# Kernel tuning notes

Measured on AMD Instinct MI355X. Metric: run time of the kernel, lower is better.

## Reference

```python
import jax, jax.numpy as jnp
import numpy as np

H, D = 8, 64          # num_heads, head_dim
DM = 512              # model/feature dim for q,k,v,pos
B, N, M = 8, 1024, 1024


def relative_shift(x):
    # x: [B, H, N, M] -> Transformer-XL pad/reshape shift trick
    b, h, n, m = x.shape
    x = jnp.pad(x, ((0, 0), (0, 0), (0, 0), (1, 0)))      # [B,H,N,M+1]
    x = x.reshape(b, h, m + 1, n)
    x = x[:, :, 1:, :].reshape(b, h, n, m)
    return x


def setup_inputs() -> dict:
    key = jax.random.key(0)
    ks = jax.random.split(key, 11)
    s = 0.05  # small init scale for numerical stability (glorot-ish)
    return {
        "query": jax.random.normal(ks[0], (B, N, DM), jnp.float32),
        "key": jax.random.normal(ks[1], (B, M, DM), jnp.float32),
        "value": jax.random.normal(ks[2], (B, M, DM), jnp.float32),
        "pos": jax.random.normal(ks[3], (B, M, DM), jnp.float32),
        "query_kernel": jax.random.normal(ks[4], (H, DM, D), jnp.float32) * s,
        "key_kernel": jax.random.normal(ks[5], (H, DM, D), jnp.float32) * s,
        "value_kernel": jax.random.normal(ks[6], (H, DM, D), jnp.float32) * s,
        "pos_kernel": jax.random.normal(ks[7], (H, DM, D), jnp.float32) * s,
        "projection_kernel": jax.random.normal(ks[8], (H, D, DM), jnp.float32) * s,
        "pos_bias_u": jax.random.normal(ks[9], (H, D), jnp.float32) * s,
        "pos_bias_v": jax.random.normal(ks[10], (H, D), jnp.float32) * s,
    }


def reference(query, key, value, pos, query_kernel, key_kernel, value_kernel,
              pos_kernel, projection_kernel, pos_bias_u, pos_bias_v):
    # per-head projections
    q = jnp.einsum("bni,hid->bnhd", query, query_kernel)
    k = jnp.einsum("bmi,hid->bmhd", key, key_kernel)
    v = jnp.einsum("bmi,hid->bmhd", value, value_kernel)
    p = jnp.einsum("bmi,hid->bmhd", pos, pos_kernel)

    q_u = q + pos_bias_u  # broadcast [H,D] over [B,N,H,D]
    q_v = q + pos_bias_v

    logits_u = jnp.einsum("bnhd,bmhd->bhnm", q_u, k)
    logits_v = relative_shift(jnp.einsum("bnhd,bmhd->bhnm", q_v, p))

    m = logits_u.shape[3]
    logits = (logits_u + logits_v[:, :, :, :m]) / jnp.sqrt(
        jnp.asarray(D, logits_u.dtype))

    attn = jax.nn.softmax(logits, axis=-1)            # [B,H,N,M]
    ctx = jnp.einsum("bhnm,bmhd->bnhd", attn, v)      # [B,N,H,D]
    out = jnp.einsum("bnhd,hdo->bno", ctx, projection_kernel)
    return out
```

## Files before the change

kernel.cpp:

```cpp
#include <hip/hip_runtime.h>
#include <hip/hip_bf16.h>
#include <math.h>

#define SB 8
#define SS 1024
#define SDM 512
#define SH 8
#define SD 64

typedef unsigned short ushort;
typedef __attribute__((ext_vector_type(8))) short bf16x8;
typedef __attribute__((ext_vector_type(4))) float f32x4;

#define MFMA16(a, b, c) __builtin_amdgcn_mfma_f32_16x16x32_bf16(a, b, c, 0, 0, 0)

static __device__ __forceinline__ ushort f2b(float f) {
    union { float f; unsigned u; } v; v.f = f;
    unsigned r = v.u + 0x7FFF + ((v.u >> 16) & 1);
    return (ushort)(r >> 16);
}

static __device__ __forceinline__ void gll16(const void* g, void* l) {
    __builtin_amdgcn_global_load_lds(
        (const __attribute__((address_space(1))) unsigned int*)g,
        (__attribute__((address_space(3))) unsigned int*)l, 16, 0, 0);
}

__global__ __launch_bounds__(256) void convert_x_kernel(
    const float* __restrict__ q, const float* __restrict__ k,
    const float* __restrict__ v, const float* __restrict__ p,
    ushort* __restrict__ xbf)
{
    const int which = blockIdx.y;
    const float* src = (which == 0) ? q : (which == 1) ? k : (which == 2) ? v : p;
    ushort* dst = xbf + (size_t)which * ((size_t)SB * SS * SDM);
    size_t i = ((size_t)blockIdx.x * 256 + threadIdx.x) * 8;
    float4 a = *(const float4*)(src + i);
    float4 b = *(const float4*)(src + i + 4);
    union { ushort u[8]; uint4 v4; } o;
    o.u[0] = f2b(a.x); o.u[1] = f2b(a.y); o.u[2] = f2b(a.z); o.u[3] = f2b(a.w);
    o.u[4] = f2b(b.x); o.u[5] = f2b(b.y); o.u[6] = f2b(b.z); o.u[7] = f2b(b.w);
    *(uint4*)(dst + i) = o.v4;
}

__global__ __launch_bounds__(256) void convert_w_kernel(
    const float* __restrict__ qw, const float* __restrict__ kw,
    const float* __restrict__ vw, const float* __restrict__ pw,
    const float* __restrict__ projw, ushort* __restrict__ wt)
{
    const int which = blockIdx.y;
    const int idx = blockIdx.x * 256 + threadIdx.x;
    const int c  = idx >> 9;
    const int kk = idx & 511;
    float val;
    if (which < 4) {
        const float* W = (which == 0) ? qw : (which == 1) ? kw : (which == 2) ? vw : pw;
        const int h = c >> 6, d = c & 63;
        val = W[(size_t)h * SDM * SD + (size_t)kk * SD + d];
    } else {
        val = projw[(size_t)kk * SDM + c];
    }
    wt[(size_t)which * SDM * SDM + (size_t)c * SDM + kk] = f2b(val);
}

__global__ __launch_bounds__(256) void projmm_kernel(
    const ushort* __restrict__ xbf, const ushort* __restrict__ wt,
    const float* __restrict__ bias_u, const float* __restrict__ bias_v,
    ushort* __restrict__ quo, ushort* __restrict__ qvo,
    ushort* __restrict__ ko, ushort* __restrict__ po,
    ushort* __restrict__ vto)
{
    __shared__ ushort Asm[128 * 32];
    __shared__ ushort Bsm[128 * 32];

    const int tid  = threadIdx.x;
    const int wave = tid >> 6, lane = tid & 63;
    const int quad = lane >> 4, l15 = lane & 15;
    const int which = blockIdx.z;
    const int row0 = blockIdx.x * 128;
    const int col0 = blockIdx.y * 128;
    const int wr = wave >> 1, wc = wave & 1;

    const ushort* A  = xbf + (size_t)which * ((size_t)SB * SS * SDM) + (size_t)row0 * SDM;
    const ushort* Bw = wt  + (size_t)which * (SDM * SDM) + (size_t)col0 * SDM;

    f32x4 acc[4][4];
#pragma unroll
    for (int i = 0; i < 4; ++i)
#pragma unroll
        for (int j = 0; j < 4; ++j) acc[i][j] = (f32x4){0.f, 0.f, 0.f, 0.f};

    for (int k0 = 0; k0 < SDM; k0 += 32) {
#pragma unroll
        for (int j = 0; j < 2; ++j) {
            int t = j * 256 + tid;
            int r = t >> 2, kp = (t & 3) * 8;
            gll16(A  + (size_t)r * SDM + k0 + kp, (char*)Asm + t * 16);
            gll16(Bw + (size_t)r * SDM + k0 + kp, (char*)Bsm + t * 16);
        }
        __syncthreads();

        bf16x8 af[4], bfr[4];
#pragma unroll
        for (int mt = 0; mt < 4; ++mt)
            af[mt] = *(const bf16x8*)&Asm[(wr * 64 + mt * 16 + l15) * 32 + quad * 8];
#pragma unroll
        for (int nt = 0; nt < 4; ++nt)
            bfr[nt] = *(const bf16x8*)&Bsm[(wc * 64 + nt * 16 + l15) * 32 + quad * 8];
#pragma unroll
        for (int mt = 0; mt < 4; ++mt)
#pragma unroll
            for (int nt = 0; nt < 4; ++nt)
                acc[mt][nt] = MFMA16(af[mt], bfr[nt], acc[mt][nt]);
        __syncthreads();
    }

    const float SC = 0.125f;
#pragma unroll
    for (int nt = 0; nt < 4; ++nt) {
        const int C = col0 + wc * 64 + nt * 16 + l15;
        const int h = C >> 6, d = C & 63;
        if (which == 0) {
            const float bu = bias_u[C];
            const float bv = bias_v[C];
#pragma unroll
            for (int mt = 0; mt < 4; ++mt) {
                const int Rb = row0 + wr * 64 + mt * 16 + quad * 4;
                const int b = Rb >> 10;
                const int n = Rb & 1023;
                const size_t base = ((size_t)(b * SH + h) * SS + n) * SD + d;
#pragma unroll
                for (int r = 0; r < 4; ++r) {
                    quo[base + (size_t)r * SD] = f2b((acc[mt][nt][r] + bu) * SC);
                    qvo[base + (size_t)r * SD] = f2b((acc[mt][nt][r] + bv) * SC);
                }
            }
        } else if (which == 1 || which == 3) {
            ushort* out = (which == 1) ? ko : po;
#pragma unroll
            for (int mt = 0; mt < 4; ++mt) {
                const int Rb = row0 + wr * 64 + mt * 16 + quad * 4;
                const int b = Rb >> 10;
                const int n = Rb & 1023;
                const size_t base = ((size_t)(b * SH + h) * SS + n) * SD + d;
#pragma unroll
                for (int r = 0; r < 4; ++r)
                    out[base + (size_t)r * SD] = f2b(acc[mt][nt][r]);
            }
        } else {
#pragma unroll
            for (int mt = 0; mt < 4; ++mt) {
                const int Rb = row0 + wr * 64 + mt * 16 + quad * 4;
                const int b = Rb >> 10;
                const int n = Rb & 1023;
                union { ushort u[4]; uint2 v2; } pk;
#pragma unroll
                for (int r = 0; r < 4; ++r) pk.u[r] = f2b(acc[mt][nt][r]);
                const size_t base = (size_t)(b * SH + h) * SS * SD
                                  + ((size_t)((n >> 6) * 64 + d)) * 64 + (n & 63);
                *(uint2*)&vto[base] = pk.v2;
            }
        }
    }
}

static __device__ __forceinline__ bf16x8 sfrag(const ushort* buf, int row, int seg) {
    return *(const bf16x8*)&buf[(size_t)row * 64 + ((seg ^ (row & 7)) * 8)];
}

__global__ __launch_bounds__(256) void attn_kernel(
    const ushort* __restrict__ qu, const ushort* __restrict__ qv,
    const ushort* __restrict__ kk, const ushort* __restrict__ pp,
    const ushort* __restrict__ vt, ushort* __restrict__ ctx)
{
    __shared__ ushort Kb[64 * 64];
    __shared__ ushort Pb[128 * 64];
    __shared__ float  Glds[4][16][80];
    __shared__ ushort Plds[4][16][72];

    const int tid  = threadIdx.x;
    const int wave = tid >> 6;
    const int lane = tid & 63;
    const int quad = lane >> 4;
    const int l15  = lane & 15;

    const int id   = blockIdx.x;
    const int xcd  = id & 7;
    const int slot = id >> 3;
    const int bhid = xcd * 8 + (slot >> 4);
    const int nt   = slot & 15;
    const int b    = bhid >> 3;
    const int h    = bhid & 7;
    const int n0   = nt * 64;

    const size_t bh   = (size_t)(b * SH + h);
    const ushort* qu_bh = qu + bh * SS * SD;
    const ushort* qv_bh = qv + bh * SS * SD;
    const ushort* k_bh  = kk + bh * SS * SD;
    const ushort* p_bh  = pp + bh * SS * SD;
    const ushort* vt_bh = vt + bh * SS * SD;

    const int mcD = n0 >> 6;

    const int arow  = n0 + wave * 16 + l15;
    const int arow2 = (arow + 1 < SS) ? arow + 1 : SS - 1;

    bf16x8 a_u0  = *(const bf16x8*)(qu_bh + (size_t)arow  * SD + quad * 8);
    bf16x8 a_u1  = *(const bf16x8*)(qu_bh + (size_t)arow  * SD + quad * 8 + 32);
    bf16x8 a_vl0 = *(const bf16x8*)(qv_bh + (size_t)arow  * SD + quad * 8);
    bf16x8 a_vl1 = *(const bf16x8*)(qv_bh + (size_t)arow  * SD + quad * 8 + 32);
    bf16x8 a_vu0 = *(const bf16x8*)(qv_bh + (size_t)arow2 * SD + quad * 8);
    bf16x8 a_vu1 = *(const bf16x8*)(qv_bh + (size_t)arow2 * SD + quad * 8 + 32);

    float lsum[4] = {0.f, 0.f, 0.f, 0.f};
    f32x4 O[4];
#pragma unroll
    for (int dt = 0; dt < 4; ++dt) O[dt] = (f32x4){0.f, 0.f, 0.f, 0.f};

    float  (*Gl)[80] = Glds[wave];
    ushort (*Pl)[72] = Plds[wave];

    auto stage = [&](int mc) {
        const int m0s = mc * 64;
        const int cb  = (mc <= mcD) ? (m0s - n0 + 960) : (m0s - n0 - 65);
#pragma unroll
        for (int it = 0; it < 2; ++it) {
            int t = it * 256 + tid;
            int r = t >> 3, s = t & 7;
            gll16(k_bh + (size_t)(m0s + r) * 64 + ((s ^ (r & 7)) * 8),
                  (char*)Kb + t * 16);
        }
#pragma unroll
        for (int it = 0; it < 4; ++it) {
            int t = it * 256 + tid;
            int r = t >> 3, s = t & 7;
            int c = cb + r; c = (c < 0) ? 0 : (c > SS - 1 ? SS - 1 : c);
            gll16(p_bh + (size_t)c * 64 + ((s ^ (r & 7)) * 8),
                  (char*)Pb + t * 16);
        }
    };

    stage(0);

    for (int mc = 0; mc < 16; ++mc) {
        const int m0 = mc * 64;
        const int diff = m0 - n0;
        const bool lowerband = (mc <= mcD);

        __syncthreads();

        f32x4 S[4];
#pragma unroll
        for (int mt = 0; mt < 4; ++mt) {
            const int r = mt * 16 + l15;
            f32x4 c = (f32x4){0.f, 0.f, 0.f, 0.f};
            c = MFMA16(a_u0, sfrag(Kb, r, quad), c);
            c = MFMA16(a_u1, sfrag(Kb, r, quad + 4), c);
            S[mt] = c;
        }

        float sv[4][4];
#pragma unroll
        for (int mt = 0; mt < 4; ++mt)
#pragma unroll
            for (int r = 0; r < 4; ++r) sv[mt][r] = 0.f;

        {
            const bf16x8 av0 = lowerband ? a_vl0 : a_vu0;
            const bf16x8 av1 = lowerband ? a_vl1 : a_vu1;
#pragma unroll
            for (int ti = 0; ti < 5; ++ti) {
                const int t = (3 - wave + ti) * 16 + l15;
                f32x4 g = (f32x4){0.f, 0.f, 0.f, 0.f};
                g = MFMA16(av0, sfrag(Pb, t, quad), g);
                g = MFMA16(av1, sfrag(Pb, t, quad + 4), g);
#pragma unroll
                for (int r = 0; r < 4; ++r)
                    Gl[quad * 4 + r][ti * 16 + l15] = g[r];
            }
#pragma unroll
            for (int mt = 0; mt < 4; ++mt) {
                const int mloc = mt * 16 + l15;
#pragma unroll
                for (int r = 0; r < 4; ++r) {
                    const int q4r = quad * 4 + r;
                    const int d1 = diff + mloc - (wave * 16 + q4r);
                    const bool use = lowerband ? (d1 <= 0) : (d1 >= 2);
                    if (use) sv[mt][r] = Gl[q4r][mloc - q4r + 15];
                }
            }
        }

        if (mc == mcD) {
            const int cbase = diff - 65;
            bf16x8 pu0[5], pu1[5];
#pragma unroll
            for (int ti = 0; ti < 5; ++ti) {
                int t = (3 - wave + ti) * 16 + l15;
                int c = cbase + t;
                c = (c < 0) ? 0 : (c > SS - 1 ? SS - 1 : c);
                const ushort* pr = p_bh + (size_t)c * SD + quad * 8;
                pu0[ti] = *(const bf16x8*)pr;
                pu1[ti] = *(const bf16x8*)(pr + 32);
            }
#pragma unroll
            for (int ti = 0; ti < 5; ++ti) {
                f32x4 g = (f32x4){0.f, 0.f, 0.f, 0.f};
                g = MFMA16(a_vu0, pu0[ti], g);
                g = MFMA16(a_vu1, pu1[ti], g);
#pragma unroll
                for (int r = 0; r < 4; ++r)
                    Gl[quad * 4 + r][ti * 16 + l15] = g[r];
            }
#pragma unroll
            for (int mt = 0; mt < 4; ++mt) {
                const int mloc = mt * 16 + l15;
#pragma unroll
                for (int r = 0; r < 4; ++r) {
                    const int q4r = quad * 4 + r;
                    const int d1 = diff + mloc - (wave * 16 + q4r);
                    if (d1 >= 2) sv[mt][r] = Gl[q4r][mloc - q4r + 15];
                }
            }
        }

        __syncthreads();
        if (mc + 1 < 16) stage(mc + 1);

        bf16x8 vb0[4], vb1[4];
#pragma unroll
        for (int dt = 0; dt < 4; ++dt) {
            const ushort* vp = vt_bh + (size_t)(m0 + dt * 16 + l15) * 64 + quad * 8;
            vb0[dt] = *(const bf16x8*)vp;
            vb1[dt] = *(const bf16x8*)(vp + 32);
        }

        float e[4][4];
#pragma unroll
        for (int mt = 0; mt < 4; ++mt)
#pragma unroll
            for (int r = 0; r < 4; ++r) {
                e[mt][r] = __expf(S[mt][r] + sv[mt][r]);
                lsum[r] += e[mt][r];
            }

#pragma unroll
        for (int mt = 0; mt < 4; ++mt)
#pragma unroll
            for (int r = 0; r < 4; ++r)
                Pl[quad * 4 + r][mt * 16 + l15] = f2b(e[mt][r]);

        bf16x8 ap0 = *(const bf16x8*)&Pl[l15][quad * 8];
        bf16x8 ap1 = *(const bf16x8*)&Pl[l15][32 + quad * 8];
#pragma unroll
        for (int dt = 0; dt < 4; ++dt) {
            O[dt] = MFMA16(ap0, vb0[dt], O[dt]);
            O[dt] = MFMA16(ap1, vb1[dt], O[dt]);
        }
    }

#pragma unroll
    for (int mask = 1; mask <= 8; mask <<= 1)
#pragma unroll
        for (int r = 0; r < 4; ++r)
            lsum[r] += __shfl_xor(lsum[r], mask, 16);

    float inv[4];
#pragma unroll
    for (int r = 0; r < 4; ++r) inv[r] = 1.f / lsum[r];

#pragma unroll
    for (int dt = 0; dt < 4; ++dt)
#pragma unroll
        for (int r = 0; r < 4; ++r) {
            int nn = n0 + wave * 16 + quad * 4 + r;
            ctx[((size_t)b * SS + nn) * (SH * SD) + h * SD + dt * 16 + l15] =
                f2b(O[dt][r] * inv[r]);
        }
}

__global__ __launch_bounds__(256) void outproj_kernel(
    const ushort* __restrict__ ctx, const ushort* __restrict__ wt,
    float* __restrict__ out)
{
    __shared__ ushort Asm[128 * 32];
    __shared__ ushort Bsm[128 * 32];

    const int tid  = threadIdx.x;
    const int wave = tid >> 6, lane = tid & 63;
    const int quad = lane >> 4, l15 = lane & 15;
    const int row0 = blockIdx.x * 128;
    const int col0 = blockIdx.y * 128;
    const int wr = wave >> 1, wc = wave & 1;

    const ushort* A  = ctx + (size_t)row0 * SDM;
    const ushort* Bw = wt + (size_t)4 * (SDM * SDM) + (size_t)col0 * SDM;

    f32x4 acc[4][4];
#pragma unroll
    for (int i = 0; i < 4; ++i)
#pragma unroll
        for (int j = 0; j < 4; ++j) acc[i][j] = (f32x4){0.f, 0.f, 0.f, 0.f};

    for (int k0 = 0; k0 < SDM; k0 += 32) {
#pragma unroll
        for (int j = 0; j < 2; ++j) {
            int t = j * 256 + tid;
            int r = t >> 2, kp = (t & 3) * 8;
            gll16(A  + (size_t)r * SDM + k0 + kp, (char*)Asm + t * 16);
            gll16(Bw + (size_t)r * SDM + k0 + kp, (char*)Bsm + t * 16);
        }
        __syncthreads();

        bf16x8 af[4], bfr[4];
#pragma unroll
        for (int mt = 0; mt < 4; ++mt)
            af[mt] = *(const bf16x8*)&Asm[(wr * 64 + mt * 16 + l15) * 32 + quad * 8];
#pragma unroll
        for (int nt = 0; nt < 4; ++nt)
            bfr[nt] = *(const bf16x8*)&Bsm[(wc * 64 + nt * 16 + l15) * 32 + quad * 8];
#pragma unroll
        for (int mt = 0; mt < 4; ++mt)
#pragma unroll
            for (int nt = 0; nt < 4; ++nt)
                acc[mt][nt] = MFMA16(af[mt], bfr[nt], acc[mt][nt]);
        __syncthreads();
    }

#pragma unroll
    for (int mt = 0; mt < 4; ++mt)
#pragma unroll
        for (int nt = 0; nt < 4; ++nt) {
            const int R = row0 + wr * 64 + mt * 16 + quad * 4;
            const int C = col0 + wc * 64 + nt * 16 + l15;
#pragma unroll
            for (int r = 0; r < 4; ++r)
                out[(size_t)(R + r) * SDM + C] = acc[mt][nt][r];
        }
}

extern "C" void kernel_launch(void* const* d_in, const int* in_sizes, int n_in,
                              void* d_out, int out_size, void* d_ws, size_t ws_size,
                              hipStream_t stream)
{
    const float* query  = (const float*)d_in[0];
    const float* key    = (const float*)d_in[1];
    const float* value  = (const float*)d_in[2];
    const float* pos    = (const float*)d_in[3];
    const float* qw     = (const float*)d_in[4];
    const float* kw     = (const float*)d_in[5];
    const float* vw     = (const float*)d_in[6];
    const float* pw     = (const float*)d_in[7];
    const float* projw  = (const float*)d_in[8];
    const float* bias_u = (const float*)d_in[9];
    const float* bias_v = (const float*)d_in[10];

    char* w = (char*)d_ws;
    const size_t MB = 1024 * 1024;
    ushort* xbf = (ushort*)w;
    ushort* quo = (ushort*)(w + 32 * MB);
    ushort* qvo = (ushort*)(w + 40 * MB);
    ushort* ko  = (ushort*)(w + 48 * MB);
    ushort* po  = (ushort*)(w + 56 * MB);
    ushort* vto = (ushort*)(w + 64 * MB);
    ushort* wt  = (ushort*)(w + 72 * MB);
    ushort* ctx = (ushort*)w;

    dim3 gcx(2048, 4);
    convert_x_kernel<<<gcx, 256, 0, stream>>>(query, key, value, pos, xbf);
    dim3 gcw(1024, 5);
    convert_w_kernel<<<gcw, 256, 0, stream>>>(qw, kw, vw, pw, projw, wt);

    dim3 g1(64, 4, 4);
    projmm_kernel<<<g1, 256, 0, stream>>>(xbf, wt, bias_u, bias_v,
                                          quo, qvo, ko, po, vto);

    attn_kernel<<<dim3(1024), 256, 0, stream>>>(quo, qvo, ko, po, vto, ctx);

    dim3 g3(64, 4);
    outproj_kernel<<<g3, 256, 0, stream>>>(ctx, wt, (float*)d_out);
}
```

Measured before the change: 270.4 us.

## Drop LDS staging of K/P tiles; load MFMA operands directly from global

Removes the shared-memory staging of K and shifted-P tiles via global_load_lds along with the two block-wide barriers per iteration. Each wave now reads its MFMA B operands straight from global memory (through L1/L2) and computes the clamped P row index inline. The Glds row pitch goes from 80 to 81 floats to reduce LDS bank conflicts on the scatter/gather of shifted logits. The change removes barrier stalls and LDS traffic, but the four waves now fetch overlapping P rows redundantly and load latency is no longer hidden by prefetching the next tile.

```diff
diff --git a/kernel.cpp b/kernel.cpp
--- a/kernel.cpp
+++ b/kernel.cpp
@@ -164,18 +164,12 @@
     }
 }
 
-static __device__ __forceinline__ bf16x8 sfrag(const ushort* buf, int row, int seg) {
-    return *(const bf16x8*)&buf[(size_t)row * 64 + ((seg ^ (row & 7)) * 8)];
-}
-
 __global__ __launch_bounds__(256) void attn_kernel(
     const ushort* __restrict__ qu, const ushort* __restrict__ qv,
     const ushort* __restrict__ kk, const ushort* __restrict__ pp,
     const ushort* __restrict__ vt, ushort* __restrict__ ctx)
 {
-    __shared__ ushort Kb[64 * 64];
-    __shared__ ushort Pb[128 * 64];
-    __shared__ float  Glds[4][16][80];
+    __shared__ float  Glds[4][16][81];
     __shared__ ushort Plds[4][16][72];
 
     const int tid  = threadIdx.x;
@@ -217,63 +211,37 @@
 #pragma unroll
     for (int dt = 0; dt < 4; ++dt) O[dt] = (f32x4){0.f, 0.f, 0.f, 0.f};
 
-    float  (*Gl)[80] = Glds[wave];
+    float  (*Gl)[81] = Glds[wave];
     ushort (*Pl)[72] = Plds[wave];
-
-    auto stage = [&](int mc) {
-        const int m0s = mc * 64;
-        const int cb  = (mc <= mcD) ? (m0s - n0 + 960) : (m0s - n0 - 65);
-#pragma unroll
-        for (int it = 0; it < 2; ++it) {
-            int t = it * 256 + tid;
-            int r = t >> 3, s = t & 7;
-            gll16(k_bh + (size_t)(m0s + r) * 64 + ((s ^ (r & 7)) * 8),
-                  (char*)Kb + t * 16);
-        }
-#pragma unroll
-        for (int it = 0; it < 4; ++it) {
-            int t = it * 256 + tid;
-            int r = t >> 3, s = t & 7;
-            int c = cb + r; c = (c < 0) ? 0 : (c > SS - 1 ? SS - 1 : c);
-            gll16(p_bh + (size_t)c * 64 + ((s ^ (r & 7)) * 8),
-                  (char*)Pb + t * 16);
-        }
-    };
-
-    stage(0);
 
     for (int mc = 0; mc < 16; ++mc) {
         const int m0 = mc * 64;
         const int diff = m0 - n0;
         const bool lowerband = (mc <= mcD);
 
-        __syncthreads();
-
         f32x4 S[4];
 #pragma unroll
         for (int mt = 0; mt < 4; ++mt) {
-            const int r = mt * 16 + l15;
+            const ushort* kr = k_bh + (size_t)(m0 + mt * 16 + l15) * SD + quad * 8;
             f32x4 c = (f32x4){0.f, 0.f, 0.f, 0.f};
-            c = MFMA16(a_u0, sfrag(Kb, r, quad), c);
-            c = MFMA16(a_u1, sfrag(Kb, r, quad + 4), c);
+            c = MFMA16(a_u0, *(const bf16x8*)kr, c);
+            c = MFMA16(a_u1, *(const bf16x8*)(kr + 32), c);
             S[mt] = c;
         }
 
         float sv[4][4];
-#pragma unroll
-        for (int mt = 0; mt < 4; ++mt)
-#pragma unroll
-            for (int r = 0; r < 4; ++r) sv[mt][r] = 0.f;
-
         {
             const bf16x8 av0 = lowerband ? a_vl0 : a_vu0;
             const bf16x8 av1 = lowerband ? a_vl1 : a_vu1;
+            const int cb = lowerband ? (diff + 960) : (diff - 65);
 #pragma unroll
             for (int ti = 0; ti < 5; ++ti) {
                 const int t = (3 - wave + ti) * 16 + l15;
+                int c = cb + t; c = (c < 0) ? 0 : (c > SS - 1 ? SS - 1 : c);
+                const ushort* pr = p_bh + (size_t)c * SD + quad * 8;
                 f32x4 g = (f32x4){0.f, 0.f, 0.f, 0.f};
-                g = MFMA16(av0, sfrag(Pb, t, quad), g);
-                g = MFMA16(av1, sfrag(Pb, t, quad + 4), g);
+                g = MFMA16(av0, *(const bf16x8*)pr, g);
+                g = MFMA16(av1, *(const bf16x8*)(pr + 32), g);
 #pragma unroll
                 for (int r = 0; r < 4; ++r)
                     Gl[quad * 4 + r][ti * 16 + l15] = g[r];
@@ -286,28 +254,21 @@
                     const int q4r = quad * 4 + r;
                     const int d1 = diff + mloc - (wave * 16 + q4r);
                     const bool use = lowerband ? (d1 <= 0) : (d1 >= 2);
-                    if (use) sv[mt][r] = Gl[q4r][mloc - q4r + 15];
+                    sv[mt][r] = use ? Gl[q4r][mloc - q4r + 15] : 0.f;
                 }
             }
         }
 
         if (mc == mcD) {
             const int cbase = diff - 65;
-            bf16x8 pu0[5], pu1[5];
 #pragma unroll
             for (int ti = 0; ti < 5; ++ti) {
-                int t = (3 - wave + ti) * 16 + l15;
-                int c = cbase + t;
-                c = (c < 0) ? 0 : (c > SS - 1 ? SS - 1 : c);
+                const int t = (3 - wave + ti) * 16 + l15;
+                int c = cbase + t; c = (c < 0) ? 0 : (c > SS - 1 ? SS - 1 : c);
                 const ushort* pr = p_bh + (size_t)c * SD + quad * 8;
-                pu0[ti] = *(const bf16x8*)pr;
-                pu1[ti] = *(const bf16x8*)(pr + 32);
-            }
-#pragma unroll
-            for (int ti = 0; ti < 5; ++ti) {
                 f32x4 g = (f32x4){0.f, 0.f, 0.f, 0.f};
-                g = MFMA16(a_vu0, pu0[ti], g);
-                g = MFMA16(a_vu1, pu1[ti], g);
+                g = MFMA16(a_vu0, *(const bf16x8*)pr, g);
+                g = MFMA16(a_vu1, *(const bf16x8*)(pr + 32), g);
 #pragma unroll
                 for (int r = 0; r < 4; ++r)
                     Gl[quad * 4 + r][ti * 16 + l15] = g[r];
@@ -323,9 +284,6 @@
                 }
             }
         }
-
-        __syncthreads();
-        if (mc + 1 < 16) stage(mc + 1);
 
         bf16x8 vb0[4], vb1[4];
 #pragma unroll
```

Measured after the change: 423.5 us. 1.57x slower.
